# Kernel tuning notes

Measured on AMD Instinct MI355X. Metric: run time of the kernel, lower is better.

## Reference

```python
import jax, jax.numpy as jnp
from jax import lax
import numpy as np

D_STATE = 16
D_CONV = 4
GROUPS = 4
TOKEN = 8


def group_norm(x, w, b, groups, eps=1e-5):
    # x: [B, C, H, W]; torch GroupNorm semantics
    B, C, H, W = x.shape
    xg = x.reshape(B, groups, C // groups, H, W)
    mu = xg.mean(axis=(2, 3, 4), keepdims=True)
    var = ((xg - mu) ** 2).mean(axis=(2, 3, 4), keepdims=True)
    xg = (xg - mu) / jnp.sqrt(var + eps)
    return xg.reshape(B, C, H, W) * w[None, :, None, None] + b[None, :, None, None]


def mamba_fwd(x, in_w, conv_w, conv_b, xproj_w, dt_w, dt_b, A_log, D, out_w):
    # x: [B, L, d_model]. Faithful mamba_ssm Mamba forward (no biases on in/out proj).
    Bsz, L, _ = x.shape
    d_inner = in_w.shape[0] // 2
    dt_rank = dt_w.shape[1]
    xz = x @ in_w.T                                   # [B, L, 2*d_inner]
    xi, z = jnp.split(xz, 2, axis=-1)
    # causal depthwise conv1d (kernel D_CONV) + SiLU
    xc = lax.conv_general_dilated(
        xi.transpose(0, 2, 1), conv_w, window_strides=(1,),
        padding=[(D_CONV - 1, 0)], dimension_numbers=("NCH", "OIH", "NCH"),
        feature_group_count=d_inner)
    xc = jax.nn.silu(xc + conv_b[None, :, None]).transpose(0, 2, 1)  # [B, L, d_inner]
    xdb = xc @ xproj_w.T                               # [B, L, dt_rank + 2*d_state]
    dt, Bm, Cm = jnp.split(xdb, [dt_rank, dt_rank + D_STATE], axis=-1)
    dt = jax.nn.softplus(dt @ dt_w.T + dt_b)           # [B, L, d_inner]
    A = -jnp.exp(A_log)                                # [d_inner, d_state]
    dA = jnp.exp(dt[..., None] * A)                    # [B, L, d_inner, d_state]
    dBx = dt[..., None] * Bm[:, :, None, :] * xc[..., None]

    def step(h, inp):
        dA_t, dBx_t, C_t = inp                         # [B,di,ds],[B,di,ds],[B,ds]
        h = dA_t * h + dBx_t
        y = jnp.einsum('bds,bs->bd', h, C_t)
        return h, y

    h0 = jnp.zeros((Bsz, d_inner, D_STATE), dtype=x.dtype)
    _, ys = lax.scan(step, h0, (dA.transpose(1, 0, 2, 3),
                                dBx.transpose(1, 0, 2, 3),
                                Cm.transpose(1, 0, 2)))
    y = ys.transpose(1, 0, 2) + xc * D                 # skip term D*x
    y = y * jax.nn.silu(z)
    return y @ out_w.T


def setup_inputs() -> dict:
    key = jax.random.key(0)
    ks = iter(jax.random.split(key, 48))

    def rn(shape, s=0.02):
        return jax.random.normal(next(ks), shape, dtype=jnp.float32) * s

    B, C, H, W = 4, 64, 64, 64
    inp = {"x": jax.random.normal(next(ks), (B, C, H, W), dtype=jnp.float32)}

    def mamba_params(prefix, d_model):
        d_inner = 2 * d_model
        dt_rank = -(-d_model // 16)
        inp[prefix + "_in_w"] = rn((2 * d_inner, d_model))
        inp[prefix + "_conv_w"] = rn((d_inner, 1, D_CONV))
        inp[prefix + "_conv_b"] = rn((d_inner,))
        inp[prefix + "_xproj_w"] = rn((dt_rank + 2 * D_STATE, d_inner))
        inp[prefix + "_dt_w"] = rn((d_inner, dt_rank))
        inp[prefix + "_dt_b"] = rn((d_inner,)) + 0.5
        inp[prefix + "_A_log"] = jnp.log(jnp.tile(jnp.arange(1, D_STATE + 1, dtype=jnp.float32), (d_inner, 1)))
        inp[prefix + "_D"] = jnp.ones((d_inner,), jnp.float32)
        inp[prefix + "_out_w"] = rn((d_model, d_inner))

    mamba_params("spa", C)
    mamba_params("spe", -(-C // TOKEN))  # group_channel_num = ceil(64/8) = 8
    inp["spa_gn_w"] = jnp.ones((C,), jnp.float32)
    inp["spa_gn_b"] = jnp.zeros((C,), jnp.float32)
    inp["spe_gn_w"] = jnp.ones((C,), jnp.float32)
    inp["spe_gn_b"] = jnp.zeros((C,), jnp.float32)
    inp["att_w"] = jnp.full((2,), 0.5, jnp.float32)
    return inp


def reference(x,
              spa_in_w, spa_conv_w, spa_conv_b, spa_xproj_w, spa_dt_w, spa_dt_b,
              spa_A_log, spa_D, spa_out_w,
              spe_in_w, spe_conv_w, spe_conv_b, spe_xproj_w, spe_dt_w, spe_dt_b,
              spe_A_log, spe_D, spe_out_w,
              spa_gn_w, spa_gn_b, spe_gn_w, spe_gn_b, att_w):
    B, C, H, W = x.shape
    gcn = -(-C // TOKEN)  # C == TOKEN*gcn here, so no padding path is taken

    # --- SpaMamba: flatten all pixels into one sequence [1, B*H*W, C] ---
    xs = x.transpose(0, 2, 3, 1).reshape(1, -1, C)
    ys = mamba_fwd(xs, spa_in_w, spa_conv_w, spa_conv_b, spa_xproj_w,
                   spa_dt_w, spa_dt_b, spa_A_log, spa_D, spa_out_w)
    ys = ys.reshape(B, H, W, C).transpose(0, 3, 1, 2)
    spa = jax.nn.silu(group_norm(ys, spa_gn_w, spa_gn_b, GROUPS)) + x

    # --- SpeMamba: per-pixel spectral tokens [B*H*W, TOKEN, gcn] ---
    xe = x.transpose(0, 2, 3, 1).reshape(B * H * W, TOKEN, gcn)
    ye = mamba_fwd(xe, spe_in_w, spe_conv_w, spe_conv_b, spe_xproj_w,
                   spe_dt_w, spe_dt_b, spe_A_log, spe_D, spe_out_w)
    ye = ye.reshape(B, H, W, C).transpose(0, 3, 1, 2)
    spe = x + jax.nn.silu(group_norm(ye, spe_gn_w, spe_gn_b, GROUPS))

    w = jax.nn.softmax(att_w)
    return spa * w[0] + spe * w[1] + x
```

## Files before the change

kernel.cpp:

```cpp
#include <hip/hip_runtime.h>

__device__ __forceinline__ float siluf(float x){ return x / (1.f + __expf(-x)); }
__device__ __forceinline__ float softplusf(float x){
    return fmaxf(x, 0.f) + __logf(1.f + __expf(-fabsf(x)));
}
#if __has_builtin(__builtin_amdgcn_exp2f)
__device__ __forceinline__ float fexp2(float x){ return __builtin_amdgcn_exp2f(x); }
#else
__device__ __forceinline__ float fexp2(float x){ return exp2f(x); }
#endif

__global__ void __launch_bounds__(256) k_ip1(const float* __restrict__ x,
        const float* __restrict__ in_w, const float* __restrict__ cw, const float* __restrict__ cb,
        const float* __restrict__ xpw, const float* __restrict__ dtw, const float* __restrict__ dtb,
        const float* __restrict__ A_log,
        float* __restrict__ xc, float* __restrict__ zb,
        float* __restrict__ Pb, float* __restrict__ Qb){
    __shared__ float sxc[2048];
    __shared__ float sbm[256];
    __shared__ __align__(16) float dtr[64];
    __shared__ float sxe[11][68];
    const int tid = threadIdx.x;
    const int ch = blockIdx.x;
    {
        float wr[64];
        const float4* w4 = (const float4*)(in_w + tid*64);
        #pragma unroll
        for (int k = 0; k < 16; ++k){
            float4 v = w4[k];
            wr[4*k]=v.x; wr[4*k+1]=v.y; wr[4*k+2]=v.z; wr[4*k+3]=v.w;
        }
        float cw0=0.f,cw1=0.f,cw2=0.f,cw3=0.f,cbd=0.f;
        if (tid < 128){
            cw0 = cw[tid*4+0]; cw1 = cw[tid*4+1];
            cw2 = cw[tid*4+2]; cw3 = cw[tid*4+3];
            cbd = cb[tid];
        }
        for (int pass = 0; pass < 2; ++pass){
            int l0 = ch*16 + pass*8;
            #pragma unroll
            for (int it = 0; it < 3; ++it){
                int idx = it*256 + tid;
                if (idx < 704){
                    int r = idx >> 6, c = idx & 63;
                    int p = l0 - 3 + r;
                    float v = 0.f;
                    if (p >= 0) v = x[(size_t)(p >> 12)*262144 + c*4096 + (p & 4095)];
                    sxe[r][c] = v;
                }
            }
            __syncthreads();
            if (tid < 128){
                float acc[11];
                #pragma unroll
                for (int r = 0; r < 11; ++r) acc[r] = 0.f;
                #pragma unroll
                for (int k = 0; k < 16; ++k){
                    #pragma unroll
                    for (int r = 0; r < 11; ++r){
                        float4 v = *(const float4*)&sxe[r][4*k];
                        acc[r] = fmaf(v.x, wr[4*k],   acc[r]);
                        acc[r] = fmaf(v.y, wr[4*k+1], acc[r]);
                        acc[r] = fmaf(v.z, wr[4*k+2], acc[r]);
                        acc[r] = fmaf(v.w, wr[4*k+3], acc[r]);
                    }
                }
                #pragma unroll
                for (int r = 0; r < 8; ++r){
                    float a = fmaf(cw0, acc[r],   cbd);
                    a = fmaf(cw1, acc[r+1], a);
                    a = fmaf(cw2, acc[r+2], a);
                    a = fmaf(cw3, acc[r+3], a);
                    float v = siluf(a);
                    sxc[(pass*8+r)*128 + tid] = v;
                    xc[(size_t)(l0+r)*128 + tid] = v;
                }
            } else {
                float acc[8];
                #pragma unroll
                for (int r = 0; r < 8; ++r) acc[r] = 0.f;
                #pragma unroll
                for (int k = 0; k < 16; ++k){
                    #pragma unroll
                    for (int r = 0; r < 8; ++r){
                        float4 v = *(const float4*)&sxe[r+3][4*k];
                        acc[r] = fmaf(v.x, wr[4*k],   acc[r]);
                        acc[r] = fmaf(v.y, wr[4*k+1], acc[r]);
                        acc[r] = fmaf(v.z, wr[4*k+2], acc[r]);
                        acc[r] = fmaf(v.w, wr[4*k+3], acc[r]);
                    }
                }
                int dz = tid - 128;
                #pragma unroll
                for (int r = 0; r < 8; ++r) zb[(size_t)(l0+r)*128 + dz] = acc[r];
            }
            __syncthreads();
        }
    }
    {
        int j = tid & 63, tg = tid >> 6;
        if (j < 20){
            const float4* w4  = (const float4*)(xpw + j*128);
            const float4* xc4 = (const float4*)sxc + tg*128;
            float acc[4];
            #pragma unroll
            for (int r = 0; r < 4; ++r) acc[r] = 0.f;
            #pragma unroll 8
            for (int k = 0; k < 32; ++k){
                float4 w = w4[k];
                #pragma unroll
                for (int r = 0; r < 4; ++r){
                    float4 v = xc4[r*32 + k];
                    acc[r] = fmaf(v.x, w.x, acc[r]);
                    acc[r] = fmaf(v.y, w.y, acc[r]);
                    acc[r] = fmaf(v.z, w.z, acc[r]);
                    acc[r] = fmaf(v.w, w.w, acc[r]);
                }
            }
            if (j < 4){
                #pragma unroll
                for (int r = 0; r < 4; ++r) dtr[(tg*4+r)*4 + j] = acc[r];
            } else {
                #pragma unroll
                for (int r = 0; r < 4; ++r) sbm[(tg*4+r)*16 + (j-4)] = acc[r];
            }
        }
    }
    __syncthreads();
    const int d  = tid & 127;
    const int sh = tid >> 7;
    float A8[8];
    {
        const float4* al4 = (const float4*)(A_log + d*16 + sh*8);
        float4 v0 = al4[0], v1 = al4[1];
        A8[0]=-__expf(v0.x)*1.44269504f; A8[1]=-__expf(v0.y)*1.44269504f;
        A8[2]=-__expf(v0.z)*1.44269504f; A8[3]=-__expf(v0.w)*1.44269504f;
        A8[4]=-__expf(v1.x)*1.44269504f; A8[5]=-__expf(v1.y)*1.44269504f;
        A8[6]=-__expf(v1.z)*1.44269504f; A8[7]=-__expf(v1.w)*1.44269504f;
    }
    float4 dw = *(const float4*)(dtw + d*4);
    float dbd = dtb[d];
    float P[8], Q[8];
    #pragma unroll
    for (int s = 0; s < 8; ++s){ P[s] = 1.f; Q[s] = 0.f; }
    #pragma unroll 4
    for (int i = 0; i < 16; ++i){
        float4 dt4 = *(const float4*)(dtr + i*4);
        float dv = dbd;
        dv = fmaf(dt4.x, dw.x, dv);
        dv = fmaf(dt4.y, dw.y, dv);
        dv = fmaf(dt4.z, dw.z, dv);
        dv = fmaf(dt4.w, dw.w, dv);
        float dt = softplusf(dv);
        float db = dt * sxc[i*128 + d];
        const float4* bmr = (const float4*)(sbm + i*16 + sh*8);
        float4 b0 = bmr[0], b1 = bmr[1];
        float bv[8] = {b0.x,b0.y,b0.z,b0.w,b1.x,b1.y,b1.z,b1.w};
        #pragma unroll
        for (int s = 0; s < 8; ++s){
            float a = fexp2(dt*A8[s]);
            P[s] *= a;
            Q[s] = fmaf(a, Q[s], db*bv[s]);
        }
    }
    float* Pp = Pb + (size_t)ch*2048 + d*16 + sh*8;
    float* Qp = Qb + (size_t)ch*2048 + d*16 + sh*8;
    ((float4*)Pp)[0] = make_float4(P[0],P[1],P[2],P[3]);
    ((float4*)Pp)[1] = make_float4(P[4],P[5],P[6],P[7]);
    ((float4*)Qp)[0] = make_float4(Q[0],Q[1],Q[2],Q[3]);
    ((float4*)Qp)[1] = make_float4(Q[4],Q[5],Q[6],Q[7]);
}

#define XE_   0
#define XCL_  1216
#define BCL_  3904
#define DTV_  8640
#define SPG_  8768
#define WEIN_ 8800
#define WECW_ 9056
#define WECB_ 9120
#define WEAL_ 9136
#define WDTW_ 9392
#define WDTB_ 9408
#define WDV_  9424
__global__ void __launch_bounds__(256) k_spe(
        const float* __restrict__ x,
        const float* __restrict__ ein_w, const float* __restrict__ ecw, const float* __restrict__ ecb,
        const float* __restrict__ expw, const float* __restrict__ edtw, const float* __restrict__ edtb,
        const float* __restrict__ eA_log, const float* __restrict__ eDv, const float* __restrict__ eow,
        float* __restrict__ ye, float* __restrict__ sp)
{
    __shared__ float smem[9440];
    const int tid = threadIdx.x;
    const int pix = tid >> 4;
    const int d   = tid & 15;
    const int eb  = blockIdx.x;
    const int p0  = eb * 16;
    const int b   = p0 >> 12;
    const int hw0 = p0 & 4095;

    #pragma unroll
    for (int it = 0; it < 3; ++it){
        int idx = it*256 + tid;
        if (idx < 640){
            float v;
            if      (idx < 256) v = ein_w[idx];
            else if (idx < 320) v = ecw[idx-256];
            else if (idx < 336) v = ecb[idx-320];
            else if (idx < 592) v = eA_log[idx-336];
            else if (idx < 608) v = edtw[idx-592];
            else if (idx < 624) v = edtb[idx-608];
            else                v = eDv[idx-624];
            smem[WEIN_ + idx] = v;
        }
    }
    const float* xb = x + b*262144 + hw0;
    #pragma unroll
    for (int it = 0; it < 4; ++it){
        int idx = it*256 + tid;
        smem[XE_ + (idx&15)*76 + (idx>>4)] = xb[(idx>>4)*4096 + (idx&15)];
    }
    __syncthreads();

    float wi[8], wz[8];
    #pragma unroll
    for (int g = 0; g < 8; ++g){ wi[g] = smem[WEIN_ + d*8+g]; wz[g] = smem[WEIN_ + 128 + d*8+g]; }
    float xi[8], zz[8];
    {
        const float4* xe4 = (const float4*)(smem + XE_ + pix*76);
        #pragma unroll
        for (int t = 0; t < 8; ++t){
            float4 a = xe4[t*2], bq = xe4[t*2+1];
            float xv8[8] = {a.x,a.y,a.z,a.w,bq.x,bq.y,bq.z,bq.w};
            float ai = 0.f, az = 0.f;
            #pragma unroll
            for (int g = 0; g < 8; ++g){
                ai = fmaf(xv8[g], wi[g], ai);
                az = fmaf(xv8[g], wz[g], az);
            }
            xi[t] = ai; zz[t] = az;
        }
    }
    float c0 = smem[WECW_ + d*4+0], c1 = smem[WECW_ + d*4+1];
    float c2 = smem[WECW_ + d*4+2], c3 = smem[WECW_ + d*4+3];
    float cbd = smem[WECB_ + d];
    float xcr[8];
    #pragma unroll
    for (int t = 0; t < 8; ++t){
        float a = fmaf(c3, xi[t], cbd);
        if (t >= 1) a = fmaf(c2, xi[t-1], a);
        if (t >= 2) a = fmaf(c1, xi[t-2], a);
        if (t >= 3) a = fmaf(c0, xi[t-3], a);
        xcr[t] = siluf(a);
        smem[XCL_ + pix*168 + t*20 + d] = xcr[t];
    }
    __syncthreads();

    {
        const int row = tid & 127;
        const int jh  = tid >> 7;
        const int px2 = row >> 3;
        const int t2  = row & 7;
        const float4* xr = (const float4*)(smem + XCL_ + px2*168 + t2*20);
        float4 r0 = xr[0], r1 = xr[1], r2 = xr[2], r3 = xr[3];
        float xv[16] = {r0.x,r0.y,r0.z,r0.w, r1.x,r1.y,r1.z,r1.w,
                        r2.x,r2.y,r2.z,r2.w, r3.x,r3.y,r3.z,r3.w};
        const float* wbase = expw + (1 + jh*16)*16;
        float outv[16];
        #pragma unroll
        for (int s = 0; s < 16; ++s){
            const float* wr = wbase + s*16;
            float a = 0.f;
            #pragma unroll
            for (int k = 0; k < 16; ++k) a = fmaf(xv[k], wr[k], a);
            outv[s] = a;
        }
        float4* dst4 = (float4*)(smem + BCL_ + px2*296 + t2*36 + jh*16);
        dst4[0] = make_float4(outv[0], outv[1], outv[2], outv[3]);
        dst4[1] = make_float4(outv[4], outv[5], outv[6], outv[7]);
        dst4[2] = make_float4(outv[8], outv[9], outv[10],outv[11]);
        dst4[3] = make_float4(outv[12],outv[13],outv[14],outv[15]);
        if (jh == 0){
            float accd = 0.f;
            #pragma unroll
            for (int k = 0; k < 16; ++k) accd = fmaf(xv[k], expw[k], accd);
            smem[DTV_ + px2*8 + t2] = accd;
        }
    }
    __syncthreads();

    float A16[16];
    #pragma unroll
    for (int s = 0; s < 16; ++s) A16[s] = -__expf(smem[WEAL_ + d*16+s]) * 1.44269504f;
    float dwd = smem[WDTW_ + d], dbd = smem[WDTB_ + d], Dd = smem[WDV_ + d];
    float h[16];
    #pragma unroll
    for (int s = 0; s < 16; ++s) h[s] = 0.f;
    #pragma unroll
    for (int t = 0; t < 8; ++t){
        float dtd = softplusf(fmaf(smem[DTV_ + pix*8 + t], dwd, dbd));
        float db = dtd * xcr[t];
        const float4* bc4 = (const float4*)(smem + BCL_ + pix*296 + t*36);
        float4 b0 = bc4[0], b1 = bc4[1], b2 = bc4[2], b3 = bc4[3];
        float4 cc0 = bc4[4], cc1 = bc4[5], cc2 = bc4[6], cc3 = bc4[7];
        float bv[16] = {b0.x,b0.y,b0.z,b0.w, b1.x,b1.y,b1.z,b1.w,
                        b2.x,b2.y,b2.z,b2.w, b3.x,b3.y,b3.z,b3.w};
        float cv[16] = {cc0.x,cc0.y,cc0.z,cc0.w, cc1.x,cc1.y,cc1.z,cc1.w,
                        cc2.x,cc2.y,cc2.z,cc2.w, cc3.x,cc3.y,cc3.z,cc3.w};
        float yp = 0.f;
        #pragma unroll
        for (int s = 0; s < 16; ++s){
            float a = fexp2(dtd*A16[s]);
            h[s] = fmaf(a, h[s], db*bv[s]);
            yp = fmaf(h[s], cv[s], yp);
        }
        smem[pix*168 + t*20 + d] = (yp + xcr[t]*Dd) * siluf(zz[t]);
    }
    __syncthreads();

    {
        const int half = tid >> 7;
        const int idx7 = tid & 127;
        const int pixD = idx7 >> 3;
        const int ttD  = idx7 & 7;
        const int m0   = half*4;
        const float4* y4 = (const float4*)(smem + pixD*168 + ttD*20);
        float4 y0 = y4[0], y1 = y4[1], y2 = y4[2], y3 = y4[3];
        float ylr[16] = {y0.x,y0.y,y0.z,y0.w, y1.x,y1.y,y1.z,y1.w,
                         y2.x,y2.y,y2.z,y2.w, y3.x,y3.y,y3.z,y3.w};
        float acc[4];
        #pragma unroll
        for (int mm = 0; mm < 4; ++mm){
            const float* wr = eow + (m0+mm)*16;
            float a = 0.f;
            #pragma unroll
            for (int k = 0; k < 16; ++k) a = fmaf(ylr[k], wr[k], a);
            acc[mm] = a;
        }
        float4 o; o.x=acc[0]; o.y=acc[1]; o.z=acc[2]; o.w=acc[3];
        *(float4*)(ye + (size_t)(p0+pixD)*64 + ttD*8 + m0) = o;

        float s  = acc[0]+acc[1]+acc[2]+acc[3];
        float ss = acc[0]*acc[0]+acc[1]*acc[1]+acc[2]*acc[2]+acc[3]*acc[3];
        s += __shfl_xor(s,1);  ss += __shfl_xor(ss,1);
        s += __shfl_xor(s,8);  ss += __shfl_xor(ss,8);
        s += __shfl_xor(s,16); ss += __shfl_xor(ss,16);
        s += __shfl_xor(s,32); ss += __shfl_xor(ss,32);
        int lane = tid & 63, wv = tid >> 6;
        if ((lane & 57) == 0){
            smem[SPG_ + wv*4 + ((lane>>1)&3)] = s;
            smem[SPG_ + 16 + wv*4 + ((lane>>1)&3)] = ss;
        }
    }
    __syncthreads();
    if (tid < 4){
        int blk = eb & 255;
        float S  = smem[SPG_+0*4+tid]+smem[SPG_+1*4+tid]+smem[SPG_+2*4+tid]+smem[SPG_+3*4+tid];
        float SS = smem[SPG_+16+0*4+tid]+smem[SPG_+16+1*4+tid]+smem[SPG_+16+2*4+tid]+smem[SPG_+16+3*4+tid];
        float* dst = sp + (size_t)(((4 + b)*4 + tid)*512 + blk*2);
        dst[0] = S; dst[1] = SS;
    }
}

__global__ void __launch_bounds__(256) k_scan_p2a(const float* __restrict__ Pb,
        const float* __restrict__ Qb, float* __restrict__ Ps, float* __restrict__ Qs){
    int g = blockIdx.x*256 + threadIdx.x;
    int sup = g >> 11;
    int lane = g & 2047;
    float P = 1.f, Q = 0.f;
    for (int i = 0; i < 64; i += 8){
        float p[8], q[8];
        #pragma unroll
        for (int u = 0; u < 8; ++u){
            p[u] = Pb[(size_t)(sup*64+i+u)*2048 + lane];
            q[u] = Qb[(size_t)(sup*64+i+u)*2048 + lane];
        }
        #pragma unroll
        for (int u = 0; u < 8; ++u){
            P = p[u]*P;
            Q = fmaf(p[u], Q, q[u]);
        }
    }
    Ps[g] = P; Qs[g] = Q;
}

__global__ void __launch_bounds__(256) k_scan_p2c(const float* __restrict__ Pb,
        const float* __restrict__ Qb, const float* __restrict__ Ps,
        const float* __restrict__ Qs, float* __restrict__ Hs){
    int g = blockIdx.x*256 + threadIdx.x;
    int sup = g >> 11;
    int lane = g & 2047;
    float h = 0.f;
    for (int u = 0; u < sup; ++u){
        float p = Ps[u*2048 + lane];
        float q = Qs[u*2048 + lane];
        h = fmaf(p, h, q);
    }
    for (int i = 0; i < 64; i += 8){
        float p[8], q[8];
        #pragma unroll
        for (int u = 0; u < 8; ++u){
            p[u] = Pb[(size_t)(sup*64+i+u)*2048 + lane];
            q[u] = Qb[(size_t)(sup*64+i+u)*2048 + lane];
        }
        #pragma unroll
        for (int u = 0; u < 8; ++u){
            Hs[(size_t)(sup*64+i+u)*2048 + lane] = h;
            h = fmaf(p[u], h, q[u]);
        }
    }
}

__global__ void __launch_bounds__(256) k_scan_p3(const float* __restrict__ xc,
// ... 177 lines not shown
        const float4* bp = (const float4*)(sp + (size_t)(t*16 + b*4 + g)*512 + j*16);
        float s = 0.f, ss = 0.f;
        #pragma unroll
        for (int k = 0; k < 4; ++k){ float4 v = bp[k]; s += v.x+v.z; ss += v.y+v.w; }
        s += __shfl_xor(s,1);  ss += __shfl_xor(ss,1);
        s += __shfl_xor(s,2);  ss += __shfl_xor(ss,2);
        s += __shfl_xor(s,4);  ss += __shfl_xor(ss,4);
        s += __shfl_xor(s,8);  ss += __shfl_xor(ss,8);
        s += __shfl_xor(s,16); ss += __shfl_xor(ss,16);
        if (j == 0){
            float m = s * (1.f/65536.f);
            float v = ss * (1.f/65536.f) - m*m;
            st[combo*2]   = m;
            st[combo*2+1] = rsqrtf(v + 1e-5f);
        }
    }
    const float* ysb = ys + ((size_t)(b*4096 + hw0))*64;
    const float* yeb = ye + ((size_t)(b*4096 + hw0))*64;
    #pragma unroll
    for (int it = 0; it < 8; ++it){
        int idx = it*256 + tid;
        tys[idx>>6][idx&63] = ysb[idx];
        tye[idx>>6][idx&63] = yeb[idx];
    }
    __syncthreads();
    float a0 = attw[0], a1 = attw[1];
    float mx = fmaxf(a0, a1);
    float e0 = __expf(a0-mx), e1 = __expf(a1-mx);
    float inv = 1.f/(e0+e1);
    float w0 = e0*inv, w1 = e1*inv;
    #pragma unroll
    for (int it = 0; it < 8; ++it){
        int idx = it*256 + tid;
        int c = idx >> 5, hwi = idx & 31;
        int g = c >> 4;
        size_t gx = ((size_t)(b*64 + c))*4096 + hw0 + hwi;
        float xv = x[gx];
        float ns = (tys[hwi][c] - st[g*2])     * st[g*2+1]     * gsw[c] + gsb[c];
        float ne = (tye[hwi][c] - st[8+g*2])   * st[8+g*2+1]   * gew[c] + geb[c];
        out[gx] = w0*(siluf(ns)+xv) + w1*(xv+siluf(ne)) + xv;
    }
}

#define OFF_YS 0u
#define OFF_XC 1048832u
#define OFF_Z  3145984u
#define OFF_PB 5243136u
#define OFF_QB 7340288u
#define OFF_HS 9437440u
#define OFF_YE 11534592u
#define OFF_PS 12583168u
#define OFF_QS 12615936u
#define OFF_SP 12648704u

extern "C" void kernel_launch(void* const* d_in, const int* in_sizes, int n_in,
                              void* d_out, int out_size, void* d_ws, size_t ws_size,
                              hipStream_t stream) {
    const float* x           = (const float*)d_in[0];
    const float* spa_in_w    = (const float*)d_in[1];
    const float* spa_conv_w  = (const float*)d_in[2];
    const float* spa_conv_b  = (const float*)d_in[3];
    const float* spa_xproj_w = (const float*)d_in[4];
    const float* spa_dt_w    = (const float*)d_in[5];
    const float* spa_dt_b    = (const float*)d_in[6];
    const float* spa_A_log   = (const float*)d_in[7];
    const float* spa_D       = (const float*)d_in[8];
    const float* spa_out_w   = (const float*)d_in[9];
    const float* spe_in_w    = (const float*)d_in[10];
    const float* spe_conv_w  = (const float*)d_in[11];
    const float* spe_conv_b  = (const float*)d_in[12];
    const float* spe_xproj_w = (const float*)d_in[13];
    const float* spe_dt_w    = (const float*)d_in[14];
    const float* spe_dt_b    = (const float*)d_in[15];
    const float* spe_A_log   = (const float*)d_in[16];
    const float* spe_D       = (const float*)d_in[17];
    const float* spe_out_w   = (const float*)d_in[18];
    const float* spa_gn_w    = (const float*)d_in[19];
    const float* spa_gn_b    = (const float*)d_in[20];
    const float* spe_gn_w    = (const float*)d_in[21];
    const float* spe_gn_b    = (const float*)d_in[22];
    const float* att_w       = (const float*)d_in[23];

    float* ws  = (float*)d_ws;
    float* xc  = ws + OFF_XC;
    float* zb  = ws + OFF_Z;
    float* Pb  = ws + OFF_PB;
    float* Qb  = ws + OFF_QB;
    float* Hs  = ws + OFF_HS;
    float* Ps  = ws + OFF_PS;
    float* Qs  = ws + OFF_QS;
    float* sp  = ws + OFF_SP;
    float* ysb = ws + OFF_YS;
    float* yeb = ws + OFF_YE;
    float* out = (float*)d_out;

    k_ip1     <<<1024, 256, 0, stream>>>(x, spa_in_w, spa_conv_w, spa_conv_b,
                                         spa_xproj_w, spa_dt_w, spa_dt_b, spa_A_log,
                                         xc, zb, Pb, Qb);
    k_spe     <<<1024, 256, 0, stream>>>(x, spe_in_w, spe_conv_w, spe_conv_b, spe_xproj_w,
                                         spe_dt_w, spe_dt_b, spe_A_log, spe_D, spe_out_w,
                                         yeb, sp);
    k_scan_p2a<<<128,  256, 0, stream>>>(Pb, Qb, Ps, Qs);
    k_scan_p2c<<<128,  256, 0, stream>>>(Pb, Qb, Ps, Qs, Hs);
    k_scan_p3 <<<1024, 256, 0, stream>>>(xc, zb, spa_xproj_w, spa_dt_w, spa_dt_b,
                                         spa_A_log, spa_D, Hs, spa_out_w, ysb, sp);
    k_final   <<<512,  256, 0, stream>>>(x, ysb, yeb, sp, spa_gn_w, spa_gn_b,
                                         spe_gn_w, spe_gn_b, att_w, out);
}
```

Before: 115.0 us.

## Pre-transpose input to token-major layout and read in_proj operands directly from global

Adds a transpose kernel that writes x into a token-major buffer with three zero rows of causal padding in front. The spatial in_proj kernel then reads float4 rows straight from that buffer instead of gathering strided channel-major elements into shared memory, which drops the staging loop and two barriers per pass. The cost is an extra launch and a 4 MB round trip through the workspace. The gather moves from shared memory to L1/L2-cached global loads that each thread repeats.

New measurement: 118.2 us. 1.03x slower.

```diff
diff --git a/kernel.cpp b/kernel.cpp
--- a/kernel.cpp
+++ b/kernel.cpp
@@ -10,7 +10,29 @@
 __device__ __forceinline__ float fexp2(float x){ return exp2f(x); }
 #endif
 
-__global__ void __launch_bounds__(256) k_ip1(const float* __restrict__ x,
+__global__ void __launch_bounds__(256) k_xpose(const float* __restrict__ x, float* __restrict__ xs){
+    __shared__ float t[64][65];
+    int blk = blockIdx.x;
+    int b = blk >> 6;
+    int hw0 = (blk & 63) << 6;
+    int tid = threadIdx.x;
+    if (blk == 0 && tid < 192) xs[tid] = 0.f;
+    const float* xb = x + b*262144 + hw0;
+    #pragma unroll
+    for (int it = 0; it < 16; ++it){
+        int idx = it*256 + tid;
+        t[idx>>6][idx&63] = xb[(idx>>6)*4096 + (idx&63)];
+    }
+    __syncthreads();
+    float* xsb = xs + 192 + (size_t)(b*4096 + hw0)*64;
+    #pragma unroll
+    for (int it = 0; it < 16; ++it){
+        int idx = it*256 + tid;
+        xsb[(idx>>6)*64 + (idx&63)] = t[idx&63][idx>>6];
+    }
+}
+
+__global__ void __launch_bounds__(256) k_ip1(const float* __restrict__ xs,
         const float* __restrict__ in_w, const float* __restrict__ cw, const float* __restrict__ cb,
         const float* __restrict__ xpw, const float* __restrict__ dtw, const float* __restrict__ dtb,
         const float* __restrict__ A_log,
@@ -19,7 +41,6 @@
     __shared__ float sxc[2048];
     __shared__ float sbm[256];
     __shared__ __align__(16) float dtr[64];
-    __shared__ float sxe[11][68];
     const int tid = threadIdx.x;
     const int ch = blockIdx.x;
     {
@@ -30,35 +51,21 @@
             float4 v = w4[k];
             wr[4*k]=v.x; wr[4*k+1]=v.y; wr[4*k+2]=v.z; wr[4*k+3]=v.w;
         }
-        float cw0=0.f,cw1=0.f,cw2=0.f,cw3=0.f,cbd=0.f;
         if (tid < 128){
-            cw0 = cw[tid*4+0]; cw1 = cw[tid*4+1];
-            cw2 = cw[tid*4+2]; cw3 = cw[tid*4+3];
-            cbd = cb[tid];
-        }
-        for (int pass = 0; pass < 2; ++pass){
-            int l0 = ch*16 + pass*8;
-            #pragma unroll
-            for (int it = 0; it < 3; ++it){
-                int idx = it*256 + tid;
-                if (idx < 704){
-                    int r = idx >> 6, c = idx & 63;
-                    int p = l0 - 3 + r;
-                    float v = 0.f;
-                    if (p >= 0) v = x[(size_t)(p >> 12)*262144 + c*4096 + (p & 4095)];
-                    sxe[r][c] = v;
-                }
-            }
-            __syncthreads();
-            if (tid < 128){
+            float cw0 = cw[tid*4+0], cw1 = cw[tid*4+1], cw2 = cw[tid*4+2], cw3 = cw[tid*4+3];
+            float cbd = cb[tid];
+            #pragma unroll
+            for (int pass = 0; pass < 2; ++pass){
+                int l0 = ch*16 + pass*8;
                 float acc[11];
                 #pragma unroll
                 for (int r = 0; r < 11; ++r) acc[r] = 0.f;
+                const float4* xr = ((const float4*)xs) + (size_t)l0*16;
                 #pragma unroll
                 for (int k = 0; k < 16; ++k){
                     #pragma unroll
                     for (int r = 0; r < 11; ++r){
-                        float4 v = *(const float4*)&sxe[r][4*k];
+                        float4 v = xr[r*16 + k];
                         acc[r] = fmaf(v.x, wr[4*k],   acc[r]);
                         acc[r] = fmaf(v.y, wr[4*k+1], acc[r]);
                         acc[r] = fmaf(v.z, wr[4*k+2], acc[r]);
@@ -75,28 +82,33 @@
                     sxc[(pass*8+r)*128 + tid] = v;
                     xc[(size_t)(l0+r)*128 + tid] = v;
                 }
-            } else {
+            }
+        } else {
+            int dz = tid - 128;
+            #pragma unroll
+            for (int pass = 0; pass < 2; ++pass){
+                int l0 = ch*16 + pass*8;
                 float acc[8];
                 #pragma unroll
                 for (int r = 0; r < 8; ++r) acc[r] = 0.f;
+                const float4* xr = ((const float4*)(xs + 192)) + (size_t)l0*16;
                 #pragma unroll
                 for (int k = 0; k < 16; ++k){
                     #pragma unroll
                     for (int r = 0; r < 8; ++r){
-                        float4 v = *(const float4*)&sxe[r+3][4*k];
+                        float4 v = xr[r*16 + k];
                         acc[r] = fmaf(v.x, wr[4*k],   acc[r]);
                         acc[r] = fmaf(v.y, wr[4*k+1], acc[r]);
                         acc[r] = fmaf(v.z, wr[4*k+2], acc[r]);
                         acc[r] = fmaf(v.w, wr[4*k+3], acc[r]);
                     }
                 }
-                int dz = tid - 128;
                 #pragma unroll
                 for (int r = 0; r < 8; ++r) zb[(size_t)(l0+r)*128 + dz] = acc[r];
             }
-            __syncthreads();
-        }
-    }
+        }
+    }
+    __syncthreads();
     {
         int j = tid & 63, tg = tid >> 6;
         if (j < 20){
@@ -642,6 +654,7 @@
 #define OFF_PS 12583168u
 #define OFF_QS 12615936u
 #define OFF_SP 12648704u
+#define OFF_XS 12665088u
 
 extern "C" void kernel_launch(void* const* d_in, const int* in_sizes, int n_in,
                               void* d_out, int out_size, void* d_ws, size_t ws_size,
@@ -680,11 +693,13 @@
     float* Ps  = ws + OFF_PS;
     float* Qs  = ws + OFF_QS;
     float* sp  = ws + OFF_SP;
+    float* xs  = ws + OFF_XS;
     float* ysb = ws + OFF_YS;
     float* yeb = ws + OFF_YE;
     float* out = (float*)d_out;
 
-    k_ip1     <<<1024, 256, 0, stream>>>(x, spa_in_w, spa_conv_w, spa_conv_b,
+    k_xpose   <<<256,  256, 0, stream>>>(x, xs);
+    k_ip1     <<<1024, 256, 0, stream>>>(xs, spa_in_w, spa_conv_w, spa_conv_b,
                                          spa_xproj_w, spa_dt_w, spa_dt_b, spa_A_log,
                                          xc, zb, Pb, Qb);
     k_spe     <<<1024, 256, 0, stream>>>(x, spe_in_w, spe_conv_w, spe_conv_b, spe_xproj_w,
```

## Merge spatial chunk-scan and spectral Mamba kernels into one interleaved launch

Applied to the files above, without the earlier changes.

Combines k_ip1 (the spatial in-proj, conv and chunk-local scan) and k_spe (the full spectral Mamba) into a single kernel of 2048 blocks. Even blocks run the spatial work and odd blocks run the spectral work, sharing one shared-memory array. The two independent workloads can then run concurrently on the GPU, and one launch and one inter-kernel drain go away. The cost is that every block reserves the larger shared-memory footprint and register allocation of the heavier branch, which may lower occupancy for the lighter one.

Result: slower. 135.6 us (+17.9%).

```diff
diff --git a/kernel.cpp b/kernel.cpp
--- a/kernel.cpp
+++ b/kernel.cpp
@@ -10,167 +10,10 @@
 __device__ __forceinline__ float fexp2(float x){ return exp2f(x); }
 #endif
 
-__global__ void __launch_bounds__(256) k_ip1(const float* __restrict__ x,
-        const float* __restrict__ in_w, const float* __restrict__ cw, const float* __restrict__ cb,
-        const float* __restrict__ xpw, const float* __restrict__ dtw, const float* __restrict__ dtb,
-        const float* __restrict__ A_log,
-        float* __restrict__ xc, float* __restrict__ zb,
-        float* __restrict__ Pb, float* __restrict__ Qb){
-    __shared__ float sxc[2048];
-    __shared__ float sbm[256];
-    __shared__ __align__(16) float dtr[64];
-    __shared__ float sxe[11][68];
-    const int tid = threadIdx.x;
-    const int ch = blockIdx.x;
-    {
-        float wr[64];
-        const float4* w4 = (const float4*)(in_w + tid*64);
-        #pragma unroll
-        for (int k = 0; k < 16; ++k){
-            float4 v = w4[k];
-            wr[4*k]=v.x; wr[4*k+1]=v.y; wr[4*k+2]=v.z; wr[4*k+3]=v.w;
-        }
-        float cw0=0.f,cw1=0.f,cw2=0.f,cw3=0.f,cbd=0.f;
-        if (tid < 128){
-            cw0 = cw[tid*4+0]; cw1 = cw[tid*4+1];
-            cw2 = cw[tid*4+2]; cw3 = cw[tid*4+3];
-            cbd = cb[tid];
-        }
-        for (int pass = 0; pass < 2; ++pass){
-            int l0 = ch*16 + pass*8;
-            #pragma unroll
-            for (int it = 0; it < 3; ++it){
-                int idx = it*256 + tid;
-                if (idx < 704){
-                    int r = idx >> 6, c = idx & 63;
-                    int p = l0 - 3 + r;
-                    float v = 0.f;
-                    if (p >= 0) v = x[(size_t)(p >> 12)*262144 + c*4096 + (p & 4095)];
-                    sxe[r][c] = v;
-                }
-            }
-            __syncthreads();
-            if (tid < 128){
-                float acc[11];
-                #pragma unroll
-                for (int r = 0; r < 11; ++r) acc[r] = 0.f;
-                #pragma unroll
-                for (int k = 0; k < 16; ++k){
-                    #pragma unroll
-                    for (int r = 0; r < 11; ++r){
-                        float4 v = *(const float4*)&sxe[r][4*k];
-                        acc[r] = fmaf(v.x, wr[4*k],   acc[r]);
-                        acc[r] = fmaf(v.y, wr[4*k+1], acc[r]);
-                        acc[r] = fmaf(v.z, wr[4*k+2], acc[r]);
-                        acc[r] = fmaf(v.w, wr[4*k+3], acc[r]);
-                    }
-                }
-                #pragma unroll
-                for (int r = 0; r < 8; ++r){
-                    float a = fmaf(cw0, acc[r],   cbd);
-                    a = fmaf(cw1, acc[r+1], a);
-                    a = fmaf(cw2, acc[r+2], a);
-                    a = fmaf(cw3, acc[r+3], a);
-                    float v = siluf(a);
-                    sxc[(pass*8+r)*128 + tid] = v;
-                    xc[(size_t)(l0+r)*128 + tid] = v;
-                }
-            } else {
-                float acc[8];
-                #pragma unroll
-                for (int r = 0; r < 8; ++r) acc[r] = 0.f;
-                #pragma unroll
-                for (int k = 0; k < 16; ++k){
-                    #pragma unroll
-                    for (int r = 0; r < 8; ++r){
-                        float4 v = *(const float4*)&sxe[r+3][4*k];
-                        acc[r] = fmaf(v.x, wr[4*k],   acc[r]);
-                        acc[r] = fmaf(v.y, wr[4*k+1], acc[r]);
-                        acc[r] = fmaf(v.z, wr[4*k+2], acc[r]);
-                        acc[r] = fmaf(v.w, wr[4*k+3], acc[r]);
-                    }
-                }
-                int dz = tid - 128;
-                #pragma unroll
-                for (int r = 0; r < 8; ++r) zb[(size_t)(l0+r)*128 + dz] = acc[r];
-            }
-            __syncthreads();
-        }
-    }
-    {
-        int j = tid & 63, tg = tid >> 6;
-        if (j < 20){
-            const float4* w4  = (const float4*)(xpw + j*128);
-            const float4* xc4 = (const float4*)sxc + tg*128;
-            float acc[4];
-            #pragma unroll
-            for (int r = 0; r < 4; ++r) acc[r] = 0.f;
-            #pragma unroll 8
-            for (int k = 0; k < 32; ++k){
-                float4 w = w4[k];
-                #pragma unroll
-                for (int r = 0; r < 4; ++r){
-                    float4 v = xc4[r*32 + k];
-                    acc[r] = fmaf(v.x, w.x, acc[r]);
-                    acc[r] = fmaf(v.y, w.y, acc[r]);
-                    acc[r] = fmaf(v.z, w.z, acc[r]);
-                    acc[r] = fmaf(v.w, w.w, acc[r]);
-                }
-            }
-            if (j < 4){
-                #pragma unroll
-                for (int r = 0; r < 4; ++r) dtr[(tg*4+r)*4 + j] = acc[r];
-            } else {
-                #pragma unroll
-                for (int r = 0; r < 4; ++r) sbm[(tg*4+r)*16 + (j-4)] = acc[r];
-            }
-        }
-    }
-    __syncthreads();
-    const int d  = tid & 127;
-    const int sh = tid >> 7;
-    float A8[8];
-    {
-        const float4* al4 = (const float4*)(A_log + d*16 + sh*8);
-        float4 v0 = al4[0], v1 = al4[1];
-        A8[0]=-__expf(v0.x)*1.44269504f; A8[1]=-__expf(v0.y)*1.44269504f;
-        A8[2]=-__expf(v0.z)*1.44269504f; A8[3]=-__expf(v0.w)*1.44269504f;
-        A8[4]=-__expf(v1.x)*1.44269504f; A8[5]=-__expf(v1.y)*1.44269504f;
-        A8[6]=-__expf(v1.z)*1.44269504f; A8[7]=-__expf(v1.w)*1.44269504f;
-    }
-    float4 dw = *(const float4*)(dtw + d*4);
-    float dbd = dtb[d];
-    float P[8], Q[8];
-    #pragma unroll
-    for (int s = 0; s < 8; ++s){ P[s] = 1.f; Q[s] = 0.f; }
-    #pragma unroll 4
-    for (int i = 0; i < 16; ++i){
-        float4 dt4 = *(const float4*)(dtr + i*4);
-        float dv = dbd;
-        dv = fmaf(dt4.x, dw.x, dv);
-        dv = fmaf(dt4.y, dw.y, dv);
-        dv = fmaf(dt4.z, dw.z, dv);
-        dv = fmaf(dt4.w, dw.w, dv);
-        float dt = softplusf(dv);
-        float db = dt * sxc[i*128 + d];
-        const float4* bmr = (const float4*)(sbm + i*16 + sh*8);
-        float4 b0 = bmr[0], b1 = bmr[1];
-        float bv[8] = {b0.x,b0.y,b0.z,b0.w,b1.x,b1.y,b1.z,b1.w};
-        #pragma unroll
-        for (int s = 0; s < 8; ++s){
-            float a = fexp2(dt*A8[s]);
-            P[s] *= a;
-            Q[s] = fmaf(a, Q[s], db*bv[s]);
-        }
-    }
-    float* Pp = Pb + (size_t)ch*2048 + d*16 + sh*8;
-    float* Qp = Qb + (size_t)ch*2048 + d*16 + sh*8;
-    ((float4*)Pp)[0] = make_float4(P[0],P[1],P[2],P[3]);
-    ((float4*)Pp)[1] = make_float4(P[4],P[5],P[6],P[7]);
-    ((float4*)Qp)[0] = make_float4(Q[0],Q[1],Q[2],Q[3]);
-    ((float4*)Qp)[1] = make_float4(Q[4],Q[5],Q[6],Q[7]);
-}
-
+#define SXC2_ 0
+#define SBM2_ 2048
+#define DTR2_ 2304
+#define SXE2_ 2368
 #define XE_   0
 #define XCL_  1216
 #define BCL_  3904
@@ -183,8 +26,14 @@
 #define WDTW_ 9392
 #define WDTB_ 9408
 #define WDV_  9424
-__global__ void __launch_bounds__(256) k_spe(
+
+__global__ void __launch_bounds__(256) k_ips(
         const float* __restrict__ x,
+        const float* __restrict__ in_w, const float* __restrict__ cw, const float* __restrict__ cb,
+        const float* __restrict__ xpw, const float* __restrict__ dtw, const float* __restrict__ dtb,
+        const float* __restrict__ A_log,
+        float* __restrict__ xc, float* __restrict__ zb,
+        float* __restrict__ Pb, float* __restrict__ Qb,
         const float* __restrict__ ein_w, const float* __restrict__ ecw, const float* __restrict__ ecb,
         const float* __restrict__ expw, const float* __restrict__ edtw, const float* __restrict__ edtb,
         const float* __restrict__ eA_log, const float* __restrict__ eDv, const float* __restrict__ eow,
@@ -192,173 +41,324 @@
 {
     __shared__ float smem[9440];
     const int tid = threadIdx.x;
-    const int pix = tid >> 4;
-    const int d   = tid & 15;
-    const int eb  = blockIdx.x;
-    const int p0  = eb * 16;
-    const int b   = p0 >> 12;
-    const int hw0 = p0 & 4095;
-
-    #pragma unroll
-    for (int it = 0; it < 3; ++it){
-        int idx = it*256 + tid;
-        if (idx < 640){
-            float v;
-            if      (idx < 256) v = ein_w[idx];
-            else if (idx < 320) v = ecw[idx-256];
-            else if (idx < 336) v = ecb[idx-320];
-            else if (idx < 592) v = eA_log[idx-336];
-            else if (idx < 608) v = edtw[idx-592];
-            else if (idx < 624) v = edtb[idx-608];
-            else                v = eDv[idx-624];
-            smem[WEIN_ + idx] = v;
-        }
-    }
-    const float* xb = x + b*262144 + hw0;
-    #pragma unroll
-    for (int it = 0; it < 4; ++it){
-        int idx = it*256 + tid;
-        smem[XE_ + (idx&15)*76 + (idx>>4)] = xb[(idx>>4)*4096 + (idx&15)];
-    }
-    __syncthreads();
-
-    float wi[8], wz[8];
-    #pragma unroll
-    for (int g = 0; g < 8; ++g){ wi[g] = smem[WEIN_ + d*8+g]; wz[g] = smem[WEIN_ + 128 + d*8+g]; }
-    float xi[8], zz[8];
-    {
-        const float4* xe4 = (const float4*)(smem + XE_ + pix*76);
+    if ((blockIdx.x & 1) == 0){
+        const int ch = blockIdx.x >> 1;
+        {
+            float wr[64];
+            const float4* w4 = (const float4*)(in_w + tid*64);
+            #pragma unroll
+            for (int k = 0; k < 16; ++k){
+                float4 v = w4[k];
+                wr[4*k]=v.x; wr[4*k+1]=v.y; wr[4*k+2]=v.z; wr[4*k+3]=v.w;
+            }
+            float cw0=0.f,cw1=0.f,cw2=0.f,cw3=0.f,cbd=0.f;
+            if (tid < 128){
+                cw0 = cw[tid*4+0]; cw1 = cw[tid*4+1];
+                cw2 = cw[tid*4+2]; cw3 = cw[tid*4+3];
+                cbd = cb[tid];
+            }
+            for (int pass = 0; pass < 2; ++pass){
+                int l0 = ch*16 + pass*8;
+                #pragma unroll
+                for (int it = 0; it < 3; ++it){
+                    int idx = it*256 + tid;
+                    if (idx < 704){
+                        int r = idx >> 6, c = idx & 63;
+                        int p = l0 - 3 + r;
+                        float v = 0.f;
+                        if (p >= 0) v = x[(size_t)(p >> 12)*262144 + c*4096 + (p & 4095)];
+                        smem[SXE2_ + r*68 + c] = v;
+                    }
+                }
+                __syncthreads();
+                if (tid < 128){
+                    float acc[11];
+                    #pragma unroll
+                    for (int r = 0; r < 11; ++r) acc[r] = 0.f;
+                    #pragma unroll
+                    for (int k = 0; k < 16; ++k){
+                        #pragma unroll
+                        for (int r = 0; r < 11; ++r){
+                            float4 v = *(const float4*)&smem[SXE2_ + r*68 + 4*k];
+                            acc[r] = fmaf(v.x, wr[4*k],   acc[r]);
+                            acc[r] = fmaf(v.y, wr[4*k+1], acc[r]);
+                            acc[r] = fmaf(v.z, wr[4*k+2], acc[r]);
+                            acc[r] = fmaf(v.w, wr[4*k+3], acc[r]);
+                        }
+                    }
+                    #pragma unroll
+                    for (int r = 0; r < 8; ++r){
+                        float a = fmaf(cw0, acc[r],   cbd);
+                        a = fmaf(cw1, acc[r+1], a);
+                        a = fmaf(cw2, acc[r+2], a);
+                        a = fmaf(cw3, acc[r+3], a);
+                        float v = siluf(a);
+                        smem[SXC2_ + (pass*8+r)*128 + tid] = v;
+                        xc[(size_t)(l0+r)*128 + tid] = v;
+                    }
+                } else {
+                    float acc[8];
+                    #pragma unroll
+                    for (int r = 0; r < 8; ++r) acc[r] = 0.f;
+                    #pragma unroll
+                    for (int k = 0; k < 16; ++k){
+                        #pragma unroll
+                        for (int r = 0; r < 8; ++r){
+                            float4 v = *(const float4*)&smem[SXE2_ + (r+3)*68 + 4*k];
+                            acc[r] = fmaf(v.x, wr[4*k],   acc[r]);
+                            acc[r] = fmaf(v.y, wr[4*k+1], acc[r]);
+                            acc[r] = fmaf(v.z, wr[4*k+2], acc[r]);
+                            acc[r] = fmaf(v.w, wr[4*k+3], acc[r]);
+                        }
+                    }
+                    int dz = tid - 128;
+                    #pragma unroll
+                    for (int r = 0; r < 8; ++r) zb[(size_t)(l0+r)*128 + dz] = acc[r];
+                }
+                __syncthreads();
+            }
+        }
+        {
+            int j = tid & 63, tg = tid >> 6;
+            if (j < 20){
+                const float4* w4  = (const float4*)(xpw + j*128);
+                const float4* xc4 = (const float4*)(smem + SXC2_) + tg*128;
+                float acc[4];
+                #pragma unroll
+                for (int r = 0; r < 4; ++r) acc[r] = 0.f;
+                #pragma unroll 8
+                for (int k = 0; k < 32; ++k){
+                    float4 w = w4[k];
+                    #pragma unroll
+                    for (int r = 0; r < 4; ++r){
+                        float4 v = xc4[r*32 + k];
+                        acc[r] = fmaf(v.x, w.x, acc[r]);
+                        acc[r] = fmaf(v.y, w.y, acc[r]);
+                        acc[r] = fmaf(v.z, w.z, acc[r]);
+                        acc[r] = fmaf(v.w, w.w, acc[r]);
+                    }
+                }
+                if (j < 4){
+                    #pragma unroll
+                    for (int r = 0; r < 4; ++r) smem[DTR2_ + (tg*4+r)*4 + j] = acc[r];
+                } else {
+                    #pragma unroll
+                    for (int r = 0; r < 4; ++r) smem[SBM2_ + (tg*4+r)*16 + (j-4)] = acc[r];
+                }
+            }
+        }
+        __syncthreads();
+        const int d  = tid & 127;
+        const int sh = tid >> 7;
+        float A8[8];
+        {
+            const float4* al4 = (const float4*)(A_log + d*16 + sh*8);
+            float4 v0 = al4[0], v1 = al4[1];
+            A8[0]=-__expf(v0.x)*1.44269504f; A8[1]=-__expf(v0.y)*1.44269504f;
+            A8[2]=-__expf(v0.z)*1.44269504f; A8[3]=-__expf(v0.w)*1.44269504f;
+            A8[4]=-__expf(v1.x)*1.44269504f; A8[5]=-__expf(v1.y)*1.44269504f;
+            A8[6]=-__expf(v1.z)*1.44269504f; A8[7]=-__expf(v1.w)*1.44269504f;
+        }
+        float4 dw = *(const float4*)(dtw + d*4);
+        float dbd = dtb[d];
+        float P[8], Q[8];
+        #pragma unroll
+        for (int s = 0; s < 8; ++s){ P[s] = 1.f; Q[s] = 0.f; }
+        #pragma unroll 4
+        for (int i = 0; i < 16; ++i){
+            float4 dt4 = *(const float4*)&smem[DTR2_ + i*4];
+            float dv = dbd;
+            dv = fmaf(dt4.x, dw.x, dv);
+            dv = fmaf(dt4.y, dw.y, dv);
+            dv = fmaf(dt4.z, dw.z, dv);
+            dv = fmaf(dt4.w, dw.w, dv);
+            float dt = softplusf(dv);
+            float db = dt * smem[SXC2_ + i*128 + d];
+            const float4* bmr = (const float4*)&smem[SBM2_ + i*16 + sh*8];
+            float4 b0 = bmr[0], b1 = bmr[1];
+            float bv[8] = {b0.x,b0.y,b0.z,b0.w,b1.x,b1.y,b1.z,b1.w};
+            #pragma unroll
+            for (int s = 0; s < 8; ++s){
+                float a = fexp2(dt*A8[s]);
+                P[s] *= a;
+                Q[s] = fmaf(a, Q[s], db*bv[s]);
+            }
+        }
+        float* Pp = Pb + (size_t)ch*2048 + d*16 + sh*8;
+        float* Qp = Qb + (size_t)ch*2048 + d*16 + sh*8;
+        ((float4*)Pp)[0] = make_float4(P[0],P[1],P[2],P[3]);
+        ((float4*)Pp)[1] = make_float4(P[4],P[5],P[6],P[7]);
+        ((float4*)Qp)[0] = make_float4(Q[0],Q[1],Q[2],Q[3]);
+        ((float4*)Qp)[1] = make_float4(Q[4],Q[5],Q[6],Q[7]);
+    } else {
+        const int pix = tid >> 4;
+        const int d   = tid & 15;
+        const int eb  = blockIdx.x >> 1;
+        const int p0  = eb * 16;
+        const int b   = p0 >> 12;
+        const int hw0 = p0 & 4095;
+
+        #pragma unroll
+        for (int it = 0; it < 3; ++it){
+            int idx = it*256 + tid;
+            if (idx < 640){
+                float v;
+                if      (idx < 256) v = ein_w[idx];
+                else if (idx < 320) v = ecw[idx-256];
+                else if (idx < 336) v = ecb[idx-320];
+                else if (idx < 592) v = eA_log[idx-336];
+                else if (idx < 608) v = edtw[idx-592];
+                else if (idx < 624) v = edtb[idx-608];
+                else                v = eDv[idx-624];
+                smem[WEIN_ + idx] = v;
+            }
+        }
+        const float* xb = x + b*262144 + hw0;
+        #pragma unroll
+        for (int it = 0; it < 4; ++it){
+            int idx = it*256 + tid;
+            smem[XE_ + (idx&15)*76 + (idx>>4)] = xb[(idx>>4)*4096 + (idx&15)];
+        }
+        __syncthreads();
+
+        float wi[8], wz[8];
+        #pragma unroll
+        for (int g = 0; g < 8; ++g){ wi[g] = smem[WEIN_ + d*8+g]; wz[g] = smem[WEIN_ + 128 + d*8+g]; }
+        float xi[8], zz[8];
+        {
+            const float4* xe4 = (const float4*)(smem + XE_ + pix*76);
+            #pragma unroll
+            for (int t = 0; t < 8; ++t){
+                float4 a = xe4[t*2], bq = xe4[t*2+1];
+                float xv8[8] = {a.x,a.y,a.z,a.w,bq.x,bq.y,bq.z,bq.w};
+                float ai = 0.f, az = 0.f;
+                #pragma unroll
+                for (int g = 0; g < 8; ++g){
+                    ai = fmaf(xv8[g], wi[g], ai);
+                    az = fmaf(xv8[g], wz[g], az);
+                }
+                xi[t] = ai; zz[t] = az;
+            }
+        }
+        float c0 = smem[WECW_ + d*4+0], c1 = smem[WECW_ + d*4+1];
+        float c2 = smem[WECW_ + d*4+2], c3 = smem[WECW_ + d*4+3];
+        float cbd = smem[WECB_ + d];
+        float xcr[8];
         #pragma unroll
         for (int t = 0; t < 8; ++t){
-            float4 a = xe4[t*2], bq = xe4[t*2+1];
-            float xv8[8] = {a.x,a.y,a.z,a.w,bq.x,bq.y,bq.z,bq.w};
-            float ai = 0.f, az = 0.f;
-            #pragma unroll
-            for (int g = 0; g < 8; ++g){
-                ai = fmaf(xv8[g], wi[g], ai);
-                az = fmaf(xv8[g], wz[g], az);
-            }
-            xi[t] = ai; zz[t] = az;
-        }
-    }
-    float c0 = smem[WECW_ + d*4+0], c1 = smem[WECW_ + d*4+1];
-    float c2 = smem[WECW_ + d*4+2], c3 = smem[WECW_ + d*4+3];
-    float cbd = smem[WECB_ + d];
-    float xcr[8];
-    #pragma unroll
-    for (int t = 0; t < 8; ++t){
-        float a = fmaf(c3, xi[t], cbd);
-        if (t >= 1) a = fmaf(c2, xi[t-1], a);
-        if (t >= 2) a = fmaf(c1, xi[t-2], a);
-        if (t >= 3) a = fmaf(c0, xi[t-3], a);
-        xcr[t] = siluf(a);
-        smem[XCL_ + pix*168 + t*20 + d] = xcr[t];
-    }
-    __syncthreads();
-
-    {
-        const int row = tid & 127;
-        const int jh  = tid >> 7;
-        const int px2 = row >> 3;
-        const int t2  = row & 7;
-        const float4* xr = (const float4*)(smem + XCL_ + px2*168 + t2*20);
-        float4 r0 = xr[0], r1 = xr[1], r2 = xr[2], r3 = xr[3];
-        float xv[16] = {r0.x,r0.y,r0.z,r0.w, r1.x,r1.y,r1.z,r1.w,
-                        r2.x,r2.y,r2.z,r2.w, r3.x,r3.y,r3.z,r3.w};
-        const float* wbase = expw + (1 + jh*16)*16;
-        float outv[16];
-        #pragma unroll
-        for (int s = 0; s < 16; ++s){
-            const float* wr = wbase + s*16;
-            float a = 0.f;
-            #pragma unroll
-            for (int k = 0; k < 16; ++k) a = fmaf(xv[k], wr[k], a);
-            outv[s] = a;
-        }
-        float4* dst4 = (float4*)(smem + BCL_ + px2*296 + t2*36 + jh*16);
-        dst4[0] = make_float4(outv[0], outv[1], outv[2], outv[3]);
-        dst4[1] = make_float4(outv[4], outv[5], outv[6], outv[7]);
-        dst4[2] = make_float4(outv[8], outv[9], outv[10],outv[11]);
-        dst4[3] = make_float4(outv[12],outv[13],outv[14],outv[15]);
-        if (jh == 0){
-            float accd = 0.f;
-            #pragma unroll
-            for (int k = 0; k < 16; ++k) accd = fmaf(xv[k], expw[k], accd);
-            smem[DTV_ + px2*8 + t2] = accd;
-        }
-    }
-    __syncthreads();
-
-    float A16[16];
-    #pragma unroll
-    for (int s = 0; s < 16; ++s) A16[s] = -__expf(smem[WEAL_ + d*16+s]) * 1.44269504f;
-    float dwd = smem[WDTW_ + d], dbd = smem[WDTB_ + d], Dd = smem[WDV_ + d];
-    float h[16];
-    #pragma unroll
-    for (int s = 0; s < 16; ++s) h[s] = 0.f;
-    #pragma unroll
-    for (int t = 0; t < 8; ++t){
-        float dtd = softplusf(fmaf(smem[DTV_ + pix*8 + t], dwd, dbd));
-        float db = dtd * xcr[t];
-        const float4* bc4 = (const float4*)(smem + BCL_ + pix*296 + t*36);
-        float4 b0 = bc4[0], b1 = bc4[1], b2 = bc4[2], b3 = bc4[3];
-        float4 cc0 = bc4[4], cc1 = bc4[5], cc2 = bc4[6], cc3 = bc4[7];
-        float bv[16] = {b0.x,b0.y,b0.z,b0.w, b1.x,b1.y,b1.z,b1.w,
-                        b2.x,b2.y,b2.z,b2.w, b3.x,b3.y,b3.z,b3.w};
-        float cv[16] = {cc0.x,cc0.y,cc0.z,cc0.w, cc1.x,cc1.y,cc1.z,cc1.w,
-                        cc2.x,cc2.y,cc2.z,cc2.w, cc3.x,cc3.y,cc3.z,cc3.w};
-        float yp = 0.f;
-        #pragma unroll
-        for (int s = 0; s < 16; ++s){
-            float a = fexp2(dtd*A16[s]);
-            h[s] = fmaf(a, h[s], db*bv[s]);
-            yp = fmaf(h[s], cv[s], yp);
-        }
-        smem[pix*168 + t*20 + d] = (yp + xcr[t]*Dd) * siluf(zz[t]);
-    }
-    __syncthreads();
-
-    {
-        const int half = tid >> 7;
-        const int idx7 = tid & 127;
-        const int pixD = idx7 >> 3;
-        const int ttD  = idx7 & 7;
-        const int m0   = half*4;
-        const float4* y4 = (const float4*)(smem + pixD*168 + ttD*20);
-        float4 y0 = y4[0], y1 = y4[1], y2 = y4[2], y3 = y4[3];
-        float ylr[16] = {y0.x,y0.y,y0.z,y0.w, y1.x,y1.y,y1.z,y1.w,
-                         y2.x,y2.y,y2.z,y2.w, y3.x,y3.y,y3.z,y3.w};
-        float acc[4];
-        #pragma unroll
-        for (int mm = 0; mm < 4; ++mm){
-            const float* wr = eow + (m0+mm)*16;
-            float a = 0.f;
-            #pragma unroll
-            for (int k = 0; k < 16; ++k) a = fmaf(ylr[k], wr[k], a);
-            acc[mm] = a;
-        }
-        float4 o; o.x=acc[0]; o.y=acc[1]; o.z=acc[2]; o.w=acc[3];
-        *(float4*)(ye + (size_t)(p0+pixD)*64 + ttD*8 + m0) = o;
-
-        float s  = acc[0]+acc[1]+acc[2]+acc[3];
-        float ss = acc[0]*acc[0]+acc[1]*acc[1]+acc[2]*acc[2]+acc[3]*acc[3];
-        s += __shfl_xor(s,1);  ss += __shfl_xor(ss,1);
-        s += __shfl_xor(s,8);  ss += __shfl_xor(ss,8);
-        s += __shfl_xor(s,16); ss += __shfl_xor(ss,16);
-        s += __shfl_xor(s,32); ss += __shfl_xor(ss,32);
-        int lane = tid & 63, wv = tid >> 6;
-        if ((lane & 57) == 0){
-            smem[SPG_ + wv*4 + ((lane>>1)&3)] = s;
-            smem[SPG_ + 16 + wv*4 + ((lane>>1)&3)] = ss;
-        }
-    }
-    __syncthreads();
-    if (tid < 4){
-        int blk = eb & 255;
-        float S  = smem[SPG_+0*4+tid]+smem[SPG_+1*4+tid]+smem[SPG_+2*4+tid]+smem[SPG_+3*4+tid];
-        float SS = smem[SPG_+16+0*4+tid]+smem[SPG_+16+1*4+tid]+smem[SPG_+16+2*4+tid]+smem[SPG_+16+3*4+tid];
-        float* dst = sp + (size_t)(((4 + b)*4 + tid)*512 + blk*2);
-        dst[0] = S; dst[1] = SS;
+            float a = fmaf(c3, xi[t], cbd);
+            if (t >= 1) a = fmaf(c2, xi[t-1], a);
+            if (t >= 2) a = fmaf(c1, xi[t-2], a);
+            if (t >= 3) a = fmaf(c0, xi[t-3], a);
+            xcr[t] = siluf(a);
+            smem[XCL_ + pix*168 + t*20 + d] = xcr[t];
+        }
+        __syncthreads();
+
+        {
+            const int row = tid & 127;
+            const int jh  = tid >> 7;
+            const int px2 = row >> 3;
+            const int t2  = row & 7;
+            const float4* xr = (const float4*)(smem + XCL_ + px2*168 + t2*20);
+            float4 r0 = xr[0], r1 = xr[1], r2 = xr[2], r3 = xr[3];
+            float xv[16] = {r0.x,r0.y,r0.z,r0.w, r1.x,r1.y,r1.z,r1.w,
+                            r2.x,r2.y,r2.z,r2.w, r3.x,r3.y,r3.z,r3.w};
+            const float* wbase = expw + (1 + jh*16)*16;
+            float outv[16];
+            #pragma unroll
+            for (int s = 0; s < 16; ++s){
+                const float* wr = wbase + s*16;
+                float a = 0.f;
+                #pragma unroll
+                for (int k = 0; k < 16; ++k) a = fmaf(xv[k], wr[k], a);
+                outv[s] = a;
+            }
+            float4* dst4 = (float4*)(smem + BCL_ + px2*296 + t2*36 + jh*16);
+            dst4[0] = make_float4(outv[0], outv[1], outv[2], outv[3]);
+            dst4[1] = make_float4(outv[4], outv[5], outv[6], outv[7]);
+            dst4[2] = make_float4(outv[8], outv[9], outv[10],outv[11]);
+            dst4[3] = make_float4(outv[12],outv[13],outv[14],outv[15]);
+            if (jh == 0){
+                float accd = 0.f;
+                #pragma unroll
+                for (int k = 0; k < 16; ++k) accd = fmaf(xv[k], expw[k], accd);
+                smem[DTV_ + px2*8 + t2] = accd;
+            }
+        }
+        __syncthreads();
+
+        float A16[16];
+        #pragma unroll
+        for (int s = 0; s < 16; ++s) A16[s] = -__expf(smem[WEAL_ + d*16+s]) * 1.44269504f;
+        float dwd = smem[WDTW_ + d], dbd = smem[WDTB_ + d], Dd = smem[WDV_ + d];
+        float h[16];
+        #pragma unroll
+        for (int s = 0; s < 16; ++s) h[s] = 0.f;
+        #pragma unroll
+        for (int t = 0; t < 8; ++t){
+            float dtd = softplusf(fmaf(smem[DTV_ + pix*8 + t], dwd, dbd));
+            float db = dtd * xcr[t];
+            const float4* bc4 = (const float4*)(smem + BCL_ + pix*296 + t*36);
+            float4 b0 = bc4[0], b1 = bc4[1], b2 = bc4[2], b3 = bc4[3];
+            float4 cc0 = bc4[4], cc1 = bc4[5], cc2 = bc4[6], cc3 = bc4[7];
+            float bv[16] = {b0.x,b0.y,b0.z,b0.w, b1.x,b1.y,b1.z,b1.w,
+                            b2.x,b2.y,b2.z,b2.w, b3.x,b3.y,b3.z,b3.w};
+            float cv[16] = {cc0.x,cc0.y,cc0.z,cc0.w, cc1.x,cc1.y,cc1.z,cc1.w,
+                            cc2.x,cc2.y,cc2.z,cc2.w, cc3.x,cc3.y,cc3.z,cc3.w};
+            float yp = 0.f;
+            #pragma unroll
+            for (int s = 0; s < 16; ++s){
+                float a = fexp2(dtd*A16[s]);
+                h[s] = fmaf(a, h[s], db*bv[s]);
+                yp = fmaf(h[s], cv[s], yp);
+            }
+            smem[pix*168 + t*20 + d] = (yp + xcr[t]*Dd) * siluf(zz[t]);
+        }
+        __syncthreads();
+
+        {
+            const int half = tid >> 7;
+            const int idx7 = tid & 127;
+            const int pixD = idx7 >> 3;
+            const int ttD  = idx7 & 7;
+            const int m0   = half*4;
+            const float4* y4 = (const float4*)(smem + pixD*168 + ttD*20);
+            float4 y0 = y4[0], y1 = y4[1], y2 = y4[2], y3 = y4[3];
+            float ylr[16] = {y0.x,y0.y,y0.z,y0.w, y1.x,y1.y,y1.z,y1.w,
+                             y2.x,y2.y,y2.z,y2.w, y3.x,y3.y,y3.z,y3.w};
+            float acc[4];
+            #pragma unroll
+            for (int mm = 0; mm < 4; ++mm){
+                const float* wr = eow + (m0+mm)*16;
+                float a = 0.f;
+                #pragma unroll
+                for (int k = 0; k < 16; ++k) a = fmaf(ylr[k], wr[k], a);
+                acc[mm] = a;
+            }
+            float4 o; o.x=acc[0]; o.y=acc[1]; o.z=acc[2]; o.w=acc[3];
+            *(float4*)(ye + (size_t)(p0+pixD)*64 + ttD*8 + m0) = o;
+
+            float s  = acc[0]+acc[1]+acc[2]+acc[3];
+            float ss = acc[0]*acc[0]+acc[1]*acc[1]+acc[2]*acc[2]+acc[3]*acc[3];
+            s += __shfl_xor(s,1);  ss += __shfl_xor(ss,1);
+            s += __shfl_xor(s,8);  ss += __shfl_xor(ss,8);
+            s += __shfl_xor(s,16); ss += __shfl_xor(ss,16);
+            s += __shfl_xor(s,32); ss += __shfl_xor(ss,32);
+            int lane = tid & 63, wv = tid >> 6;
+            if ((lane & 57) == 0){
+                smem[SPG_ + wv*4 + ((lane>>1)&3)] = s;
+                smem[SPG_ + 16 + wv*4 + ((lane>>1)&3)] = ss;
+            }
+        }
+        __syncthreads();
+        if (tid < 4){
+            int blk = eb & 255;
+            float S  = smem[SPG_+0*4+tid]+smem[SPG_+1*4+tid]+smem[SPG_+2*4+tid]+smem[SPG_+3*4+tid];
+            float SS = smem[SPG_+16+0*4+tid]+smem[SPG_+16+1*4+tid]+smem[SPG_+16+2*4+tid]+smem[SPG_+16+3*4+tid];
+            float* dst = sp + (size_t)(((4 + b)*4 + tid)*512 + blk*2);
+            dst[0] = S; dst[1] = SS;
+        }
     }
 }
 
@@ -684,10 +684,10 @@
     float* yeb = ws + OFF_YE;
     float* out = (float*)d_out;
 
-    k_ip1     <<<1024, 256, 0, stream>>>(x, spa_in_w, spa_conv_w, spa_conv_b,
+    k_ips     <<<2048, 256, 0, stream>>>(x, spa_in_w, spa_conv_w, spa_conv_b,
                                          spa_xproj_w, spa_dt_w, spa_dt_b, spa_A_log,
-                                         xc, zb, Pb, Qb);
-    k_spe     <<<1024, 256, 0, stream>>>(x, spe_in_w, spe_conv_w, spe_conv_b, spe_xproj_w,
+                                         xc, zb, Pb, Qb,
+                                         spe_in_w, spe_conv_w, spe_conv_b, spe_xproj_w,
                                          spe_dt_w, spe_dt_b, spe_A_log, spe_D, spe_out_w,
                                          yeb, sp);
     k_scan_p2a<<<128,  256, 0, stream>>>(Pb, Qb, Ps, Qs);
```
